# Performance work log

Measured on AMD Instinct MI355X. Metric: run time of the kernel, lower is better.

Reference implementation:

```python
import jax, jax.numpy as jnp
import numpy as np

B, T, C, H = 4, 2048, 1024, 16  # batch, seq, embed, heads; head_dim = C // H = 64


def setup_inputs() -> dict:
    key = jax.random.key(0)
    ks = jax.random.split(key, 9)
    s = 1.0 / np.sqrt(C)
    return {
        "query": jax.random.normal(ks[0], (B, T, C), jnp.float32),
        "key": jax.random.normal(ks[1], (B, T, C), jnp.float32),
        "value": jax.random.normal(ks[2], (B, T, C), jnp.float32),
        "mask": jax.random.randint(ks[3], (1, 1, T, T), 0, 2, jnp.int32),
        "Wq": jax.random.normal(ks[4], (C, C), jnp.float32) * s,
        "Wk": jax.random.normal(ks[5], (C, C), jnp.float32) * s,
        "Wv": jax.random.normal(ks[6], (C, C), jnp.float32) * s,
        "Wp": jax.random.normal(ks[7], (C, C), jnp.float32) * s,
        "bp": jax.random.normal(ks[8], (C,), jnp.float32) * s,
    }


def reference(query, key, value, mask, Wq, Wk, Wv, Wp, bp):
    # torch Linear: y = x @ W.T (no bias for q/k/v)
    q = jnp.einsum("btc,dc->btd", query, Wq)
    k = jnp.einsum("btc,dc->btd", key, Wk)
    v = jnp.einsum("btc,dc->btd", value, Wv)
    hd = C // H
    # [B,T,C] -> [B,H,T,hd]
    q = q.reshape(B, T, H, hd).transpose(0, 2, 1, 3)
    k = k.reshape(B, T, H, hd).transpose(0, 2, 1, 3)
    v = v.reshape(B, T, H, hd).transpose(0, 2, 1, 3)
    # NOTE: scale uses FULL embed dim C (faithful to source), not head_dim.
    wei = jnp.einsum("bhqd,bhkd->bhqk", q, k) * (C ** -0.5)
    # Faithful quirk: masked positions are zero-filled (not -inf) BEFORE softmax.
    wei = jnp.where(mask == 0, jnp.zeros((), wei.dtype), wei)
    wei = jax.nn.softmax(wei, axis=-1)
    out = jnp.einsum("bhqk,bhkd->bhqd", wei, v)
    out = out.transpose(0, 2, 1, 3).reshape(B, T, C)
    # proj (dropout omitted: eval mode / p=0)
    return jnp.einsum("btc,dc->btd", out, Wp) + bp
```

## Files before the change

kernel.cpp:

```cpp
#include <hip/hip_runtime.h>
#include <hip/hip_bf16.h>
#include <cstdint>
#include <cstddef>

static constexpr int Bn = 4, Tn = 2048, Cn = 1024, Hn = 16, HD = 64;
static constexpr int Mn = Bn * Tn;
static constexpr float SCALE = 0.03125f;
static constexpr float QSCALE = 0.03125f * 1.4426950408889634f;

typedef __attribute__((ext_vector_type(8))) short s16x8;
typedef __attribute__((ext_vector_type(4))) short s16x4;
typedef __attribute__((ext_vector_type(4))) float f32x4;
typedef __attribute__((ext_vector_type(2))) unsigned u32x2;

#define DEVFN __device__ __forceinline__

DEVFN unsigned short f2bf(float f) {
  union { float f; unsigned u; } v; v.f = f;
  unsigned r = v.u + 0x7fffu + ((v.u >> 16) & 1u);
  return (unsigned short)(r >> 16);
}

DEVFN float exp2_hw(float x) {
  float r;
  asm("v_exp_f32 %0, %1" : "=v"(r) : "v"(x));
  return r;
}

DEVFN void gload_lds16(const void* g, void* l) {
  __builtin_amdgcn_global_load_lds(
      (const __attribute__((address_space(1))) void*)g,
      (__attribute__((address_space(3))) void*)l, 16, 0, 0);
}

__global__ __launch_bounds__(256) void k_prep(
    const float* __restrict__ q, const float* __restrict__ k, const float* __restrict__ v,
    const float* __restrict__ wq, const float* __restrict__ wk,
    const float* __restrict__ wv, const float* __restrict__ wp,
    const int* __restrict__ mask,
    unsigned short* __restrict__ Xq, unsigned short* __restrict__ Xk,
    unsigned short* __restrict__ Xv,
    unsigned short* __restrict__ Wqb, unsigned short* __restrict__ Wkb,
    unsigned short* __restrict__ Wvb, unsigned short* __restrict__ Wpb,
    unsigned* __restrict__ bits) {
  const int NX = (Mn * Cn / 4) / 256;
  const int NW = (Cn * Cn / 4) / 256;
  int bid = blockIdx.x, tid = threadIdx.x;
  if (bid < 3 * NX) {
    const float* src = bid < NX ? q : (bid < 2 * NX ? k : v);
    unsigned short* dst = bid < NX ? Xq : (bid < 2 * NX ? Xk : Xv);
    int i = (bid & (NX - 1)) * 256 + tid;
    float4 vv = reinterpret_cast<const float4*>(src)[i];
    ushort4 o;
    o.x = f2bf(vv.x); o.y = f2bf(vv.y); o.z = f2bf(vv.z); o.w = f2bf(vv.w);
    reinterpret_cast<ushort4*>(dst)[i] = o;
  } else if (bid < 3 * NX + 4 * NW) {
    int t = (bid - 3 * NX) / NW;
    const float* src = t == 0 ? wq : t == 1 ? wk : t == 2 ? wv : wp;
    unsigned short* dst = t == 0 ? Wqb : t == 1 ? Wkb : t == 2 ? Wvb : Wpb;
    int i = ((bid - 3 * NX) & (NW - 1)) * 256 + tid;
    float4 vv = reinterpret_cast<const float4*>(src)[i];
    ushort4 o;
    o.x = f2bf(vv.x); o.y = f2bf(vv.y); o.z = f2bf(vv.z); o.w = f2bf(vv.w);
    reinterpret_cast<ushort4*>(dst)[i] = o;
  } else {
    int i = (bid - 3 * NX - 4 * NW) * 256 + tid;
    unsigned long long b = __ballot(mask[i] != 0);
    int lane = tid & 63;
    if (lane == 0)        bits[i >> 5] = (unsigned)b;
    else if (lane == 32)  bits[i >> 5] = (unsigned)(b >> 32);
  }
}

template <bool F32OUT>
DEVFN void gemm_body(const unsigned short* __restrict__ A,
                     const unsigned short* __restrict__ Bt,
                     void* __restrict__ Cv, const float* __restrict__ bias,
                     float oscale, int bx, int by) {
  const int N = Cn, K = Cn;
  __shared__ __align__(16) char As[128 * 64 * 2];
  __shared__ __align__(16) char Bs[128 * 64 * 2];
  const int tid = threadIdx.x, lane = tid & 63, wid = tid >> 6;
  const int l15 = lane & 15, lg = lane >> 4;
  const int wm = (wid >> 1) * 64, wn = (wid & 1) * 64;
  const int m0 = by * 128, n0 = bx * 128;

  f32x4 acc[4][4];
#pragma unroll
  for (int i = 0; i < 4; ++i)
#pragma unroll
    for (int j = 0; j < 4; ++j) acc[i][j] = f32x4{0.f, 0.f, 0.f, 0.f};

  for (int k0 = 0; k0 < K; k0 += 64) {
#pragma unroll
    for (int it = 0; it < 4; ++it) {
      int chunk = it * 256 + tid;
      int row = chunk >> 3;
      int kg = (chunk & 7) ^ (row & 7);
      gload_lds16(A + (size_t)(m0 + row) * K + k0 + kg * 8,
                  As + (it * 256 + wid * 64) * 16);
      gload_lds16(Bt + (size_t)(n0 + row) * K + k0 + kg * 8,
                  Bs + (it * 256 + wid * 64) * 16);
    }
    __syncthreads();
#pragma unroll
    for (int kk = 0; kk < 64; kk += 32) {
      s16x8 a[4], b[4];
#pragma unroll
      for (int i = 0; i < 4; ++i) {
        int ra = wm + i * 16 + l15;
        a[i] = *(const s16x8*)(As + ra * 128 + (((kk + lg * 8) * 2) ^ ((ra & 7) << 4)));
        int rb = wn + i * 16 + l15;
        b[i] = *(const s16x8*)(Bs + rb * 128 + (((kk + lg * 8) * 2) ^ ((rb & 7) << 4)));
      }
#pragma unroll
      for (int i = 0; i < 4; ++i)
#pragma unroll
        for (int j = 0; j < 4; ++j)
          acc[i][j] = __builtin_amdgcn_mfma_f32_16x16x32_bf16(a[i], b[j], acc[i][j], 0, 0, 0);
    }
    __syncthreads();
  }
#pragma unroll
  for (int i = 0; i < 4; ++i)
#pragma unroll
    for (int j = 0; j < 4; ++j)
#pragma unroll
      for (int q = 0; q < 4; ++q) {
        int r = m0 + wm + i * 16 + lg * 4 + q;
        int c = n0 + wn + j * 16 + l15;
        float v = acc[i][j][q];
        if (F32OUT) ((float*)Cv)[(size_t)r * N + c] = v + bias[c];
        else        ((unsigned short*)Cv)[(size_t)r * N + c] = f2bf(v * oscale);
      }
}

DEVFN void gemm_swz(int& bx, int& by) {
  int flat = blockIdx.y * 8 + blockIdx.x;
  int swz = (flat & 7) * 64 + (flat >> 3);
  bx = swz & 7; by = swz >> 3;
}

__global__ __launch_bounds__(256) void k_gemmQKV(
    const unsigned short* __restrict__ Xq, const unsigned short* __restrict__ Xk,
    const unsigned short* __restrict__ Xv,
    const unsigned short* __restrict__ Wqb, const unsigned short* __restrict__ Wkb,
    const unsigned short* __restrict__ Wvb,
    unsigned short* __restrict__ Qb, unsigned short* __restrict__ Kb,
    unsigned short* __restrict__ Vb) {
  int z = blockIdx.z;
  const unsigned short* A  = z == 0 ? Xq : z == 1 ? Xk : Xv;
  const unsigned short* Bt = z == 0 ? Wqb : z == 1 ? Wkb : Wvb;
  unsigned short* C        = z == 0 ? Qb : z == 1 ? Kb : Vb;
  float oscale             = z == 0 ? QSCALE : 1.0f;
  int bx, by; gemm_swz(bx, by);
  gemm_body<false>(A, Bt, C, nullptr, oscale, bx, by);
}

__global__ __launch_bounds__(256) void k_gemmO(const unsigned short* __restrict__ A,
                                               const unsigned short* __restrict__ Bt,
                                               float* __restrict__ C,
                                               const float* __restrict__ bias) {
  int bx, by; gemm_swz(bx, by);
  gemm_body<true>(A, Bt, C, bias, 1.0f, bx, by);
}

__global__ __launch_bounds__(256) void k_attn(const unsigned short* __restrict__ Qg,
                                              const unsigned short* __restrict__ Kg,
                                              const unsigned short* __restrict__ Vg,
                                              const unsigned* __restrict__ mbits,
                                              unsigned short* __restrict__ Og) {
  __shared__ __align__(16) char QPs[128 * 128];
  __shared__ __align__(16) char Ks[64 * 128];
  __shared__ __align__(16) char Vts[64 * 128];
  __shared__ unsigned Mw[128 * 2];
  __shared__ float Ls[128];

  const int tid = threadIdx.x, lane = tid & 63, wid = tid >> 6;
  const int l15 = lane & 15, lg = lane >> 4;
  const int qt = blockIdx.x, bh = blockIdx.y;
  const int b = bh >> 4, h = bh & 15;
  const size_t rowbase = (size_t)b * Tn;
  const int cbase = h * 64;

  const int dp = lane & 31;
  const int g  = wid * 2 + (lane >> 5);
  const int qrm = tid >> 1, wmi = tid & 1;

#pragma unroll
  for (int it = 0; it < 4; ++it) {
    int chunk = it * 256 + tid;
    int row = chunk >> 3;
    int kg = (chunk & 7) ^ (row & 7);
    gload_lds16(Qg + (rowbase + qt * 128 + row) * Cn + cbase + kg * 8,
                QPs + (it * 256 + wid * 64) * 16);
  }
#pragma unroll
  for (int it = 0; it < 2; ++it) {
    int chunk = it * 256 + tid;
    int row = chunk >> 3;
    int kg = (chunk & 7) ^ (row & 7);
    gload_lds16(Kg + (rowbase + row) * Cn + cbase + kg * 8,
                Ks + (it * 256 + wid * 64) * 16);
  }
  unsigned w[8];
  {
    const unsigned* vsrc = (const unsigned*)(Vg + (rowbase + g * 8) * Cn + cbase) + dp;
#pragma unroll
    for (int j = 0; j < 8; ++j) w[j] = vsrc[(size_t)j * (Cn / 2)];
  }
  unsigned mreg = mbits[(size_t)(qt * 128 + qrm) * (Tn / 32) + wmi];
  __syncthreads();

  s16x8 qf[2][2];
#pragma unroll
  for (int m = 0; m < 2; ++m)
#pragma unroll
    for (int kh = 0; kh < 2; ++kh) {
      int ra = wid * 32 + m * 16 + l15;
      qf[m][kh] = *(const s16x8*)(QPs + ra * 128 + ((kh * 64 + lg * 16) ^ ((ra & 7) << 4)));
    }
  {
    union { unsigned u[4]; s16x8 v; } lo, hi;
#pragma unroll
    for (int j = 0; j < 4; ++j) {
      lo.u[j] = __builtin_amdgcn_perm(w[2 * j + 1], w[2 * j], 0x05040100u);
      hi.u[j] = __builtin_amdgcn_perm(w[2 * j + 1], w[2 * j], 0x07060302u);
    }
    int d0 = dp * 2, swv = (dp & 7) << 4;
    *(s16x8*)(Vts + d0 * 128 + ((g * 16) ^ swv)) = lo.v;
    *(s16x8*)(Vts + (d0 + 1) * 128 + ((g * 16) ^ swv)) = hi.v;
    Mw[qrm * 2 + wmi] = mreg;
  }

  f32x4 oacc[2][4];
#pragma unroll
  for (int m = 0; m < 2; ++m)
#pragma unroll
    for (int n = 0; n < 4; ++n) oacc[m][n] = f32x4{0.f, 0.f, 0.f, 0.f};
  float lsum[2] = {0.0f, 0.0f};

  char* Pw = QPs + wid * (32 * 128);

  for (int kt = 0; kt < Tn / 64; ++kt) {
    f32x4 sacc[4][2];
#pragma unroll
    for (int n = 0; n < 4; ++n)
#pragma unroll
      for (int m = 0; m < 2; ++m) sacc[n][m] = f32x4{0.f, 0.f, 0.f, 0.f};
#pragma unroll
    for (int kk = 0; kk < 64; kk += 32) {
      s16x8 kfr[4];
#pragma unroll
      for (int n = 0; n < 4; ++n) {
        int rb = n * 16 + l15;
        kfr[n] = *(const s16x8*)(Ks + rb * 128 + (((kk + lg * 8) * 2) ^ ((rb & 7) << 4)));
      }
#pragma unroll
      for (int n = 0; n < 4; ++n)
#pragma unroll
        for (int m = 0; m < 2; ++m)
          sacc[n][m] = __builtin_amdgcn_mfma_f32_16x16x32_bf16(kfr[n], qf[m][kk >> 5],
                                                               sacc[n][m], 0, 0, 0);
    }
    __syncthreads();

    {
      int ktn = (kt + 1) & (Tn / 64 - 1);
#pragma unroll
      for (int it = 0; it < 2; ++it) {
        int chunk = it * 256 + tid;
        int row = chunk >> 3;
        int kg = (chunk & 7) ^ (row & 7);
        gload_lds16(Kg + (rowbase + ktn * 64 + row) * Cn + cbase + kg * 8,
                    Ks + (it * 256 + wid * 64) * 16);
      }
      const unsigned* vsrc =
          (const unsigned*)(Vg + (rowbase + ktn * 64 + g * 8) * Cn + cbase) + dp;
#pragma unroll
      for (int j = 0; j < 8; ++j) w[j] = vsrc[(size_t)j * (Cn / 2)];
      mreg = mbits[(size_t)(qt * 128 + qrm) * (Tn / 32) + ktn * 2 + wmi];
    }

#pragma unroll
    for (int qi = 0; qi < 2; ++qi) {
      int qr = wid * 32 + qi * 16 + l15;
      unsigned w0 = Mw[qr * 2], w1 = Mw[qr * 2 + 1];
      int qloc = qi * 16 + l15;
      unsigned swp = (unsigned)((qloc & 7) << 4);
      float psum = 0.0f;
#pragma unroll
      for (int kf = 0; kf < 4; ++kf) {
        unsigned wm_ = (kf < 2) ? w0 : w1;
        unsigned bits4 = wm_ >> ((kf & 1) * 16 + lg * 4);
        unsigned pb[4];
#pragma unroll
        for (int r = 0; r < 4; ++r) {
          int smear = (int)(bits4 << (31 - r)) >> 31;
          union { float f; unsigned u; } sv; sv.f = sacc[kf][qi][r];
          sv.u &= (unsigned)smear;
          float pv = exp2_hw(sv.f);
          psum += pv;
          union { float f; unsigned u; } pc; pc.f = pv; pb[r] = pc.u;
        }
        union { u32x2 u; s16x4 s; } pk;
        pk.u.x = __builtin_amdgcn_perm(pb[1], pb[0], 0x07060302u);
        pk.u.y = __builtin_amdgcn_perm(pb[3], pb[2], 0x07060302u);
        *(s16x4*)(Pw + qloc * 128 + (((unsigned)(kf * 32 + lg * 8)) ^ swp)) = pk.s;
      }
      lsum[qi] += psum;
    }
    asm volatile("" ::: "memory");

#pragma unroll
    for (int kk = 0; kk < 64; kk += 32) {
      s16x8 pa[2], vb[4];
#pragma unroll
      for (int m = 0; m < 2; ++m) {
        int rp = m * 16 + l15;
        pa[m] = *(const s16x8*)(Pw + rp * 128 + (((kk + lg * 8) * 2) ^ ((rp & 7) << 4)));
      }
#pragma unroll
      for (int n = 0; n < 4; ++n) {
        int rv = n * 16 + l15;
        vb[n] = *(const s16x8*)(Vts + rv * 128 + (((kk + lg * 8) * 2) ^ (((rv >> 1) & 7) << 4)));
      }
#pragma unroll
      for (int m = 0; m < 2; ++m)
#pragma unroll
        for (int n = 0; n < 4; ++n)
          oacc[m][n] = __builtin_amdgcn_mfma_f32_16x16x32_bf16(pa[m], vb[n], oacc[m][n], 0, 0, 0);
    }
    __syncthreads();

    {
      union { unsigned u[4]; s16x8 v; } lo, hi;
#pragma unroll
      for (int j = 0; j < 4; ++j) {
        lo.u[j] = __builtin_amdgcn_perm(w[2 * j + 1], w[2 * j], 0x05040100u);
        hi.u[j] = __builtin_amdgcn_perm(w[2 * j + 1], w[2 * j], 0x07060302u);
      }
      int d0 = dp * 2, swv = (dp & 7) << 4;
      *(s16x8*)(Vts + d0 * 128 + ((g * 16) ^ swv)) = lo.v;
      *(s16x8*)(Vts + (d0 + 1) * 128 + ((g * 16) ^ swv)) = hi.v;
      Mw[qrm * 2 + wmi] = mreg;
    }
  }

#pragma unroll
  for (int qi = 0; qi < 2; ++qi) {
    float v = lsum[qi];
    v += __shfl_xor(v, 16);
    v += __shfl_xor(v, 32);
    if (lg == 0) Ls[wid * 32 + qi * 16 + l15] = v;
  }
  asm volatile("" ::: "memory");

#pragma unroll
  for (int m = 0; m < 2; ++m)
#pragma unroll
    for (int q = 0; q < 4; ++q) {
      int rloc = wid * 32 + m * 16 + lg * 4 + q;
      float inv = 1.0f / Ls[rloc];
      int rg = qt * 128 + rloc;
#pragma unroll
      for (int n = 0; n < 4; ++n)
        Og[(rowbase + rg) * Cn + cbase + n * 16 + l15] = f2bf(oacc[m][n][q] * inv);
    }
}

extern "C" void kernel_launch(void* const* d_in, const int* in_sizes, int n_in,
                              void* d_out, int out_size, void* d_ws, size_t ws_size,
                              hipStream_t stream) {
  (void)in_sizes; (void)n_in; (void)out_size; (void)ws_size;
  const float* query = (const float*)d_in[0];
  const float* key_  = (const float*)d_in[1];
  const float* value = (const float*)d_in[2];
  const int*   mask  = (const int*)d_in[3];
  const float* Wq = (const float*)d_in[4];
  const float* Wk = (const float*)d_in[5];
  const float* Wv = (const float*)d_in[6];
  const float* Wp = (const float*)d_in[7];
  const float* bp = (const float*)d_in[8];

  char* ws = (char*)d_ws;
  const size_t SX = (size_t)Mn * Cn * 2;
  const size_t SW = (size_t)Cn * Cn * 2;
  unsigned short* Xq  = (unsigned short*)(ws);
  unsigned short* Xk  = (unsigned short*)(ws + SX);
  unsigned short* Xv  = (unsigned short*)(ws + 2 * SX);
  unsigned short* Wqb = (unsigned short*)(ws + 3 * SX);
  unsigned short* Wkb = (unsigned short*)(ws + 3 * SX + SW);
  unsigned short* Wvb = (unsigned short*)(ws + 3 * SX + 2 * SW);
  unsigned short* Wpb = (unsigned short*)(ws + 3 * SX + 3 * SW);
  unsigned short* Qb  = (unsigned short*)(ws + 3 * SX + 4 * SW);
  unsigned short* Kb  = (unsigned short*)(ws + 4 * SX + 4 * SW);
  unsigned short* Vb  = (unsigned short*)(ws + 5 * SX + 4 * SW);
  unsigned*       mb  = (unsigned*)(ws + 6 * SX + 4 * SW);
  unsigned short* AO  = Xq;

  const int NPREP = 3 * ((Mn * Cn / 4) / 256) + 4 * ((Cn * Cn / 4) / 256)
                    + (Tn * Tn) / 256;
  k_prep<<<dim3(NPREP), dim3(256), 0, stream>>>(query, key_, value, Wq, Wk, Wv, Wp, mask,
                                                Xq, Xk, Xv, Wqb, Wkb, Wvb, Wpb, mb);

  k_gemmQKV<<<dim3(8, 64, 3), dim3(256), 0, stream>>>(Xq, Xk, Xv, Wqb, Wkb, Wvb,
                                                      Qb, Kb, Vb);

  k_attn<<<dim3(16, 64), dim3(256), 0, stream>>>(Qb, Kb, Vb, mb, AO);

  k_gemmO<<<dim3(8, 64), dim3(256), 0, stream>>>(AO, Wpb, (float*)d_out, bp);
}
```

Measured before the change: 224.9 us.

## Fuse fp32-to-bf16 activation conversion into QKV GEMM and compute row sums via MFMA

The separate prep pass that converted the query, key and value activations to bf16 is removed. The QKV GEMM now loads fp32 activations directly, rounds them to bf16 in registers (round-half-up packing) and writes them into swizzled LDS, which saves one full write and re-read of three activation tensors. In attention, the softmax row sums come from an extra MFMA against a ones vector instead of scalar accumulation, cross-lane shuffles and an LDS array. The trade-offs are twice the global read bytes for the A operand, a synchronous register-staged load in place of direct-to-LDS loads, a slightly different rounding mode, and extra MFMA work per tile.

Measured after the change: 227.4 us. No clear change (+1.1%).

```diff
diff --git a/kernel.cpp b/kernel.cpp
--- a/kernel.cpp
+++ b/kernel.cpp
@@ -5,7 +5,6 @@
 
 static constexpr int Bn = 4, Tn = 2048, Cn = 1024, Hn = 16, HD = 64;
 static constexpr int Mn = Bn * Tn;
-static constexpr float SCALE = 0.03125f;
 static constexpr float QSCALE = 0.03125f * 1.4426950408889634f;
 
 typedef __attribute__((ext_vector_type(8))) short s16x8;
@@ -27,6 +26,12 @@
   return r;
 }
 
+DEVFN unsigned pack_bf16_rhu(float a0, float a1) {
+  union { float f; unsigned u; } x0, x1;
+  x0.f = a0; x1.f = a1;
+  return __builtin_amdgcn_perm(x1.u + 0x8000u, x0.u + 0x8000u, 0x07060302u);
+}
+
 DEVFN void gload_lds16(const void* g, void* l) {
   __builtin_amdgcn_global_load_lds(
       (const __attribute__((address_space(1))) void*)g,
@@ -34,37 +39,25 @@
 }
 
 __global__ __launch_bounds__(256) void k_prep(
-    const float* __restrict__ q, const float* __restrict__ k, const float* __restrict__ v,
     const float* __restrict__ wq, const float* __restrict__ wk,
     const float* __restrict__ wv, const float* __restrict__ wp,
     const int* __restrict__ mask,
-    unsigned short* __restrict__ Xq, unsigned short* __restrict__ Xk,
-    unsigned short* __restrict__ Xv,
     unsigned short* __restrict__ Wqb, unsigned short* __restrict__ Wkb,
     unsigned short* __restrict__ Wvb, unsigned short* __restrict__ Wpb,
     unsigned* __restrict__ bits) {
-  const int NX = (Mn * Cn / 4) / 256;
   const int NW = (Cn * Cn / 4) / 256;
   int bid = blockIdx.x, tid = threadIdx.x;
-  if (bid < 3 * NX) {
-    const float* src = bid < NX ? q : (bid < 2 * NX ? k : v);
-    unsigned short* dst = bid < NX ? Xq : (bid < 2 * NX ? Xk : Xv);
-    int i = (bid & (NX - 1)) * 256 + tid;
-    float4 vv = reinterpret_cast<const float4*>(src)[i];
-    ushort4 o;
-    o.x = f2bf(vv.x); o.y = f2bf(vv.y); o.z = f2bf(vv.z); o.w = f2bf(vv.w);
-    reinterpret_cast<ushort4*>(dst)[i] = o;
-  } else if (bid < 3 * NX + 4 * NW) {
-    int t = (bid - 3 * NX) / NW;
+  if (bid < 4 * NW) {
+    int t = bid / NW;
     const float* src = t == 0 ? wq : t == 1 ? wk : t == 2 ? wv : wp;
     unsigned short* dst = t == 0 ? Wqb : t == 1 ? Wkb : t == 2 ? Wvb : Wpb;
-    int i = ((bid - 3 * NX) & (NW - 1)) * 256 + tid;
+    int i = (bid & (NW - 1)) * 256 + tid;
     float4 vv = reinterpret_cast<const float4*>(src)[i];
     ushort4 o;
     o.x = f2bf(vv.x); o.y = f2bf(vv.y); o.z = f2bf(vv.z); o.w = f2bf(vv.w);
     reinterpret_cast<ushort4*>(dst)[i] = o;
   } else {
-    int i = (bid - 3 * NX - 4 * NW) * 256 + tid;
+    int i = (bid - 4 * NW) * 256 + tid;
     unsigned long long b = __ballot(mask[i] != 0);
     int lane = tid & 63;
     if (lane == 0)        bits[i >> 5] = (unsigned)b;
@@ -72,12 +65,109 @@
   }
 }
 
-template <bool F32OUT>
-DEVFN void gemm_body(const unsigned short* __restrict__ A,
-                     const unsigned short* __restrict__ Bt,
-                     void* __restrict__ Cv, const float* __restrict__ bias,
-                     float oscale, int bx, int by) {
-  const int N = Cn, K = Cn;
+DEVFN void gemm_swz(int& bx, int& by) {
+  int flat = blockIdx.y * 8 + blockIdx.x;
+  int swz = (flat & 7) * 64 + (flat >> 3);
+  bx = swz & 7; by = swz >> 3;
+}
+
+__global__ __launch_bounds__(256) void k_gemmQKV(
+    const float* __restrict__ Aq, const float* __restrict__ Ak,
+    const float* __restrict__ Av,
+    const unsigned short* __restrict__ Wqb, const unsigned short* __restrict__ Wkb,
+    const unsigned short* __restrict__ Wvb,
+    unsigned short* __restrict__ Qb, unsigned short* __restrict__ Kb,
+    unsigned short* __restrict__ Vb) {
+  const int K = Cn, N = Cn;
+  int z = blockIdx.z;
+  const float* A           = z == 0 ? Aq : z == 1 ? Ak : Av;
+  const unsigned short* Bt = z == 0 ? Wqb : z == 1 ? Wkb : Wvb;
+  unsigned short* C        = z == 0 ? Qb : z == 1 ? Kb : Vb;
+  float oscale             = z == 0 ? QSCALE : 1.0f;
+  int bx, by; gemm_swz(bx, by);
+
+  __shared__ __align__(16) char As[128 * 64 * 2];
+  __shared__ __align__(16) char Bs[128 * 64 * 2];
+  const int tid = threadIdx.x, lane = tid & 63, wid = tid >> 6;
+  const int l15 = lane & 15, lg = lane >> 4;
+  const int wm = (wid >> 1) * 64, wn = (wid & 1) * 64;
+  const int m0 = by * 128, n0 = bx * 128;
+
+  f32x4 acc[4][4];
+#pragma unroll
+  for (int i = 0; i < 4; ++i)
+#pragma unroll
+    for (int j = 0; j < 4; ++j) acc[i][j] = f32x4{0.f, 0.f, 0.f, 0.f};
+
+  for (int k0 = 0; k0 < K; k0 += 64) {
+#pragma unroll
+    for (int it = 0; it < 4; ++it) {
+      int chunk = it * 256 + tid;
+      int row = chunk >> 3;
+      int kg = (chunk & 7) ^ (row & 7);
+      gload_lds16(Bt + (size_t)(n0 + row) * K + k0 + kg * 8,
+                  Bs + (it * 256 + wid * 64) * 16);
+    }
+    f32x4 av[4][2];
+#pragma unroll
+    for (int it = 0; it < 4; ++it) {
+      int chunk = it * 256 + tid;
+      int row = chunk >> 3;
+      int kgc = chunk & 7;
+      const float* src = A + (size_t)(m0 + row) * K + k0 + kgc * 8;
+      av[it][0] = *(const f32x4*)(src);
+      av[it][1] = *(const f32x4*)(src + 4);
+    }
+#pragma unroll
+    for (int it = 0; it < 4; ++it) {
+      int chunk = it * 256 + tid;
+      int row = chunk >> 3;
+      int kgc = chunk & 7;
+      union { unsigned u[4]; s16x8 v; } pk;
+#pragma unroll
+      for (int h = 0; h < 2; ++h) {
+        pk.u[h * 2 + 0] = pack_bf16_rhu(av[it][h][0], av[it][h][1]);
+        pk.u[h * 2 + 1] = pack_bf16_rhu(av[it][h][2], av[it][h][3]);
+      }
+      *(s16x8*)(As + row * 128 + ((kgc * 16) ^ ((row & 7) << 4))) = pk.v;
+    }
+    __syncthreads();
+#pragma unroll
+    for (int kk = 0; kk < 64; kk += 32) {
+      s16x8 a[4], b[4];
+#pragma unroll
+      for (int i = 0; i < 4; ++i) {
+        int ra = wm + i * 16 + l15;
+        a[i] = *(const s16x8*)(As + ra * 128 + (((kk + lg * 8) * 2) ^ ((ra & 7) << 4)));
+        int rb = wn + i * 16 + l15;
+        b[i] = *(const s16x8*)(Bs + rb * 128 + (((kk + lg * 8) * 2) ^ ((rb & 7) << 4)));
+      }
+#pragma unroll
+      for (int i = 0; i < 4; ++i)
+#pragma unroll
+        for (int j = 0; j < 4; ++j)
+          acc[i][j] = __builtin_amdgcn_mfma_f32_16x16x32_bf16(a[i], b[j], acc[i][j], 0, 0, 0);
+    }
+    __syncthreads();
+  }
+#pragma unroll
+  for (int i = 0; i < 4; ++i)
+#pragma unroll
+    for (int j = 0; j < 4; ++j)
+#pragma unroll
+      for (int q = 0; q < 4; ++q) {
+        int r = m0 + wm + i * 16 + lg * 4 + q;
+        int c = n0 + wn + j * 16 + l15;
+        ((unsigned short*)C)[(size_t)r * N + c] = f2bf(acc[i][j][q] * oscale);
+      }
+}
+
+__global__ __launch_bounds__(256) void k_gemmO(const unsigned short* __restrict__ A,
+                                               const unsigned short* __restrict__ Bt,
+                                               float* __restrict__ Cv,
+                                               const float* __restrict__ bias) {
+  const int K = Cn, N = Cn;
+  int bx, by; gemm_swz(bx, by);
   __shared__ __align__(16) char As[128 * 64 * 2];
   __shared__ __align__(16) char Bs[128 * 64 * 2];
   const int tid = threadIdx.x, lane = tid & 63, wid = tid >> 6;
@@ -129,40 +219,8 @@
       for (int q = 0; q < 4; ++q) {
         int r = m0 + wm + i * 16 + lg * 4 + q;
         int c = n0 + wn + j * 16 + l15;
-        float v = acc[i][j][q];
-        if (F32OUT) ((float*)Cv)[(size_t)r * N + c] = v + bias[c];
-        else        ((unsigned short*)Cv)[(size_t)r * N + c] = f2bf(v * oscale);
-      }
-}
-
-DEVFN void gemm_swz(int& bx, int& by) {
-  int flat = blockIdx.y * 8 + blockIdx.x;
-  int swz = (flat & 7) * 64 + (flat >> 3);
-  bx = swz & 7; by = swz >> 3;
-}
-
-__global__ __launch_bounds__(256) void k_gemmQKV(
-    const unsigned short* __restrict__ Xq, const unsigned short* __restrict__ Xk,
-    const unsigned short* __restrict__ Xv,
-    const unsigned short* __restrict__ Wqb, const unsigned short* __restrict__ Wkb,
-    const unsigned short* __restrict__ Wvb,
-    unsigned short* __restrict__ Qb, unsigned short* __restrict__ Kb,
-    unsigned short* __restrict__ Vb) {
-  int z = blockIdx.z;
-  const unsigned short* A  = z == 0 ? Xq : z == 1 ? Xk : Xv;
-  const unsigned short* Bt = z == 0 ? Wqb : z == 1 ? Wkb : Wvb;
-  unsigned short* C        = z == 0 ? Qb : z == 1 ? Kb : Vb;
-  float oscale             = z == 0 ? QSCALE : 1.0f;
-  int bx, by; gemm_swz(bx, by);
-  gemm_body<false>(A, Bt, C, nullptr, oscale, bx, by);
-}
-
-__global__ __launch_bounds__(256) void k_gemmO(const unsigned short* __restrict__ A,
-                                               const unsigned short* __restrict__ Bt,
-                                               float* __restrict__ C,
-                                               const float* __restrict__ bias) {
-  int bx, by; gemm_swz(bx, by);
-  gemm_body<true>(A, Bt, C, bias, 1.0f, bx, by);
+        Cv[(size_t)r * N + c] = acc[i][j][q] + bias[c];
+      }
 }
 
 __global__ __launch_bounds__(256) void k_attn(const unsigned short* __restrict__ Qg,
@@ -174,7 +232,6 @@
   __shared__ __align__(16) char Ks[64 * 128];
   __shared__ __align__(16) char Vts[64 * 128];
   __shared__ unsigned Mw[128 * 2];
-  __shared__ float Ls[128];
 
   const int tid = threadIdx.x, lane = tid & 63, wid = tid >> 6;
   const int l15 = lane & 15, lg = lane >> 4;
@@ -238,7 +295,12 @@
   for (int m = 0; m < 2; ++m)
 #pragma unroll
     for (int n = 0; n < 4; ++n) oacc[m][n] = f32x4{0.f, 0.f, 0.f, 0.f};
-  float lsum[2] = {0.0f, 0.0f};
+  f32x4 lacc[2];
+  lacc[0] = f32x4{0.f, 0.f, 0.f, 0.f};
+  lacc[1] = f32x4{0.f, 0.f, 0.f, 0.f};
+  s16x8 vones;
+#pragma unroll
+  for (int e = 0; e < 8; ++e) vones[e] = (short)0x3F80;
 
   char* Pw = QPs + wid * (32 * 128);
 
@@ -288,7 +350,6 @@
       unsigned w0 = Mw[qr * 2], w1 = Mw[qr * 2 + 1];
       int qloc = qi * 16 + l15;
       unsigned swp = (unsigned)((qloc & 7) << 4);
-      float psum = 0.0f;
 #pragma unroll
       for (int kf = 0; kf < 4; ++kf) {
         unsigned wm_ = (kf < 2) ? w0 : w1;
@@ -299,16 +360,14 @@
           int smear = (int)(bits4 << (31 - r)) >> 31;
           union { float f; unsigned u; } sv; sv.f = sacc[kf][qi][r];
           sv.u &= (unsigned)smear;
-          float pv = exp2_hw(sv.f);
-          psum += pv;
-          union { float f; unsigned u; } pc; pc.f = pv; pb[r] = pc.u;
+          union { float f; unsigned u; } pc; pc.f = exp2_hw(sv.f);
+          pb[r] = pc.u;
         }
         union { u32x2 u; s16x4 s; } pk;
         pk.u.x = __builtin_amdgcn_perm(pb[1], pb[0], 0x07060302u);
         pk.u.y = __builtin_amdgcn_perm(pb[3], pb[2], 0x07060302u);
         *(s16x4*)(Pw + qloc * 128 + (((unsigned)(kf * 32 + lg * 8)) ^ swp)) = pk.s;
       }
-      lsum[qi] += psum;
     }
     asm volatile("" ::: "memory");
 
@@ -326,10 +385,12 @@
         vb[n] = *(const s16x8*)(Vts + rv * 128 + (((kk + lg * 8) * 2) ^ (((rv >> 1) & 7) << 4)));
       }
 #pragma unroll
-      for (int m = 0; m < 2; ++m)
+      for (int m = 0; m < 2; ++m) {
 #pragma unroll
         for (int n = 0; n < 4; ++n)
           oacc[m][n] = __builtin_amdgcn_mfma_f32_16x16x32_bf16(pa[m], vb[n], oacc[m][n], 0, 0, 0);
+        lacc[m] = __builtin_amdgcn_mfma_f32_16x16x32_bf16(pa[m], vones, lacc[m], 0, 0, 0);
+      }
     }
     __syncthreads();
 
@@ -348,21 +409,11 @@
   }
 
 #pragma unroll
-  for (int qi = 0; qi < 2; ++qi) {
-    float v = lsum[qi];
-    v += __shfl_xor(v, 16);
-    v += __shfl_xor(v, 32);
-    if (lg == 0) Ls[wid * 32 + qi * 16 + l15] = v;
-  }
-  asm volatile("" ::: "memory");
-
-#pragma unroll
   for (int m = 0; m < 2; ++m)
 #pragma unroll
     for (int q = 0; q < 4; ++q) {
-      int rloc = wid * 32 + m * 16 + lg * 4 + q;
-      float inv = 1.0f / Ls[rloc];
-      int rg = qt * 128 + rloc;
+      float inv = 1.0f / lacc[m][q];
+      int rg = qt * 128 + wid * 32 + m * 16 + lg * 4 + q;
 #pragma unroll
       for (int n = 0; n < 4; ++n)
         Og[(rowbase + rg) * Cn + cbase + n * 16 + l15] = f2bf(oacc[m][n][q] * inv);
@@ -386,9 +437,7 @@
   char* ws = (char*)d_ws;
   const size_t SX = (size_t)Mn * Cn * 2;
   const size_t SW = (size_t)Cn * Cn * 2;
-  unsigned short* Xq  = (unsigned short*)(ws);
-  unsigned short* Xk  = (unsigned short*)(ws + SX);
-  unsigned short* Xv  = (unsigned short*)(ws + 2 * SX);
+  unsigned short* AO  = (unsigned short*)(ws);
   unsigned short* Wqb = (unsigned short*)(ws + 3 * SX);
   unsigned short* Wkb = (unsigned short*)(ws + 3 * SX + SW);
   unsigned short* Wvb = (unsigned short*)(ws + 3 * SX + 2 * SW);
@@ -397,15 +446,13 @@
   unsigned short* Kb  = (unsigned short*)(ws + 4 * SX + 4 * SW);
   unsigned short* Vb  = (unsigned short*)(ws + 5 * SX + 4 * SW);
   unsigned*       mb  = (unsigned*)(ws + 6 * SX + 4 * SW);
-  unsigned short* AO  = Xq;
-
-  const int NPREP = 3 * ((Mn * Cn / 4) / 256) + 4 * ((Cn * Cn / 4) / 256)
-                    + (Tn * Tn) / 256;
-  k_prep<<<dim3(NPREP), dim3(256), 0, stream>>>(query, key_, value, Wq, Wk, Wv, Wp, mask,
-                                                Xq, Xk, Xv, Wqb, Wkb, Wvb, Wpb, mb);
-
-  k_gemmQKV<<<dim3(8, 64, 3), dim3(256), 0, stream>>>(Xq, Xk, Xv, Wqb, Wkb, Wvb,
-                                                      Qb, Kb, Vb);
+
+  const int NPREP = 4 * ((Cn * Cn / 4) / 256) + (Tn * Tn) / 256;
+  k_prep<<<dim3(NPREP), dim3(256), 0, stream>>>(Wq, Wk, Wv, Wp, mask,
+                                                Wqb, Wkb, Wvb, Wpb, mb);
+
+  k_gemmQKV<<<dim3(8, 64, 3), dim3(256), 0, stream>>>(query, key_, value,
+                                                      Wqb, Wkb, Wvb, Qb, Kb, Vb);
 
   k_attn<<<dim3(16, 64), dim3(256), 0, stream>>>(Qb, Kb, Vb, mb, AO);
 
```
